# Kernel optimization log

Measured on AMD Instinct MI355X. Metric: run time of the kernel, lower is better.

Reference implementation:

```python
import jax, jax.numpy as jnp
import numpy as np

GAMMA = 0.5
BATCH, DIM, UNITS = 16384, 512, 1024


def setup_inputs() -> dict:
    key = jax.random.key(0)
    k1, k2 = jax.random.split(key)
    inputs = jax.random.normal(k1, (BATCH, DIM), dtype=jnp.float32)
    mu = jax.random.normal(k2, (DIM, UNITS), dtype=jnp.float32)
    return {"inputs": inputs, "mu": mu}


def reference(inputs, mu):
    # Squared L2 distance from each input row to each center (column of mu):
    x_sq = jnp.sum(inputs * inputs, axis=1, keepdims=True)        # [B, 1]
    mu_sq = jnp.sum(mu * mu, axis=0, keepdims=True)               # [1, U]
    cross = inputs @ mu                                           # [B, U] GEMM
    l2 = x_sq - 2.0 * cross + mu_sq                                # [B, U]
    return jnp.exp(-GAMMA * l2)
```

## Files before the change

### kernel.cpp

```cpp
#include <hip/hip_runtime.h>
#include <hip/hip_bf16.h>

#define BATCH 16384
#define DIM   512
#define UNITS 1024

typedef float v16f __attribute__((ext_vector_type(16)));

#define APITCH 516
#define BPITCH 33

__global__ __launch_bounds__(256)
void prep_kernel(const float* __restrict__ in, const float* __restrict__ mu,
                 unsigned char* __restrict__ A8f, unsigned char* __restrict__ B8f,
                 float* __restrict__ xsq, float* __restrict__ musq) {
    __shared__ __attribute__((aligned(16))) char smem[512 * BPITCH * 4 + 1024];
    const int t  = threadIdx.x;
    const int l  = t & 63, w = t >> 6;
    const int ln = l & 31, h = l >> 5;

    if (blockIdx.x < BATCH / 32) {
        float* lds = (float*)smem;
        float* red = (float*)(smem + 32 * APITCH * 4);
        const int c = blockIdx.x;
        const float4* src = (const float4*)(in + (size_t)c * 32 * DIM);
        float4* l4 = (float4*)lds;
#pragma unroll
        for (int i = 0; i < 16; i++) {
            const int f = i * 256 + t;
            l4[(f >> 7) * (APITCH / 4) + (f & 127)] = src[f];
        }
        __syncthreads();
        float s = 0.f;
#pragma unroll
        for (int j = 0; j < 8; j++) {
            const int kw = w * 8 + j;
            const float* p = lds + ln * APITCH + kw * 16 + h * 8;
            float4 f0 = *(const float4*)p;
            float4 f1 = *(const float4*)(p + 4);
            s += f0.x * f0.x + f0.y * f0.y + f0.z * f0.z + f0.w * f0.w
               + f1.x * f1.x + f1.y * f1.y + f1.z * f1.z + f1.w * f1.w;
            int lo = __builtin_amdgcn_cvt_pk_fp8_f32(f0.x, f0.y, 0, false);
            lo     = __builtin_amdgcn_cvt_pk_fp8_f32(f0.z, f0.w, lo, true);
            int hi = __builtin_amdgcn_cvt_pk_fp8_f32(f1.x, f1.y, 0, false);
            hi     = __builtin_amdgcn_cvt_pk_fp8_f32(f1.z, f1.w, hi, true);
            *(int2*)(A8f + (((size_t)c * 32 + kw) * 64 + l) * 8) = make_int2(lo, hi);
        }
        red[ln * 8 + w * 2 + h] = s;
        __syncthreads();
        if (t < 32) {
            float a = 0.f;
#pragma unroll
            for (int i = 0; i < 8; i++) a += red[t * 8 + i];
            xsq[c * 32 + t] = a;
        }
    } else {
        float* lds = (float*)smem;
        float* red = (float*)(smem + 512 * BPITCH * 4);
        const int nb = blockIdx.x - BATCH / 32;
        const int n0 = nb * 32;
        const int col = t & 31, kg = t >> 5;
        float s = 0.f;
        for (int i = 0; i < 64; i++) {
            const int k = i * 8 + kg;
            float v = mu[(size_t)k * UNITS + n0 + col];
            s += v * v;
            lds[k * BPITCH + col] = v;
        }
        red[col * 8 + kg] = s;
        __syncthreads();
        if (t < 32) {
            float a = 0.f;
#pragma unroll
            for (int i = 0; i < 8; i++) a += red[t * 8 + i];
            musq[n0 + t] = a;
        }
#pragma unroll
        for (int j = 0; j < 8; j++) {
            const int kw = w * 8 + j;
            const float* p = lds + (kw * 16 + h * 8) * BPITCH + ln;
            float f[8];
#pragma unroll
            for (int i = 0; i < 8; i++) f[i] = p[i * BPITCH];
            int lo = __builtin_amdgcn_cvt_pk_fp8_f32(f[0], f[1], 0, false);
            lo     = __builtin_amdgcn_cvt_pk_fp8_f32(f[2], f[3], lo, true);
            int hi = __builtin_amdgcn_cvt_pk_fp8_f32(f[4], f[5], 0, false);
            hi     = __builtin_amdgcn_cvt_pk_fp8_f32(f[6], f[7], hi, true);
            *(int2*)(B8f + (((size_t)nb * 32 + kw) * 64 + l) * 8) = make_int2(lo, hi);
        }
    }
}

__global__ __launch_bounds__(256, 2)
void rbf_gemm_kernel(const unsigned char* __restrict__ A8f,
                     const unsigned char* __restrict__ B8f,
                     const float* __restrict__ xsq,
                     const float* __restrict__ musq,
                     float* __restrict__ out) {
    const int t  = threadIdx.x;
    const int l  = t & 63;
    const int w  = t >> 6;
    const int ln = l & 31;
    const int h  = l >> 5;

    const int b  = blockIdx.x;
    const int x  = b & 7;
    const int q  = b >> 3;
    const int rg = q & 15;
    const int cg = q >> 4;
    const int m0 = x * 2048 + rg * 128;
    const int ng = cg * 4 + w;
    const int chunk0 = m0 >> 5;

    const long* Af = (const long*)A8f + ((size_t)chunk0 * 32) * 64 + l;
    const long* Bf = (const long*)B8f + ((size_t)ng * 32) * 64 + l;

    v16f acc[4];
#pragma unroll
    for (int c = 0; c < 4; c++) acc[c] = (v16f)0.f;

#pragma unroll 8
    for (int kw = 0; kw < 32; kw++) {
        long bk = Bf[kw * 64];
        long a0 = Af[(0 * 32 + kw) * 64];
        long a1 = Af[(1 * 32 + kw) * 64];
        long a2 = Af[(2 * 32 + kw) * 64];
        long a3 = Af[(3 * 32 + kw) * 64];
        acc[0] = __builtin_amdgcn_mfma_f32_32x32x16_fp8_fp8(a0, bk, acc[0], 0, 0, 0);
        acc[1] = __builtin_amdgcn_mfma_f32_32x32x16_fp8_fp8(a1, bk, acc[1], 0, 0, 0);
        acc[2] = __builtin_amdgcn_mfma_f32_32x32x16_fp8_fp8(a2, bk, acc[2], 0, 0, 0);
        acc[3] = __builtin_amdgcn_mfma_f32_32x32x16_fp8_fp8(a3, bk, acc[3], 0, 0, 0);
    }

    const float mb = -0.5f * musq[ng * 32 + ln];
#pragma unroll
    for (int c = 0; c < 4; c++) {
#pragma unroll
        for (int r = 0; r < 16; r++) {
            const int rl  = (r & 3) + 8 * (r >> 2) + 4 * h;
            const int row = m0 + c * 32 + rl;
            float v = __expf(acc[c][r] - 0.5f * xsq[row] + mb);
            __builtin_nontemporal_store(v, out + (size_t)row * UNITS + ng * 32 + ln);
        }
    }
}

extern "C" void kernel_launch(void* const* d_in, const int* in_sizes, int n_in,
                              void* d_out, int out_size, void* d_ws, size_t ws_size,
                              hipStream_t stream) {
    const float* inputs = (const float*)d_in[0];
    const float* mu     = (const float*)d_in[1];
    float* out = (float*)d_out;

    char* ws = (char*)d_ws;
    unsigned char* A8f = (unsigned char*)ws;
    unsigned char* B8f = (unsigned char*)(ws + (size_t)BATCH * DIM);
    float* xsq  = (float*)(ws + (size_t)BATCH * DIM + (size_t)UNITS * DIM);
    float* musq = xsq + BATCH;

    prep_kernel<<<BATCH / 32 + UNITS / 32, 256, 0, stream>>>(
        inputs, mu, A8f, B8f, xsq, musq);
    rbf_gemm_kernel<<<1024, 256, 0, stream>>>(A8f, B8f, xsq, musq, out);
}
```

Baseline: 116.6 us.

## Use 2x2 per-wave MFMA tiles, shuffle xsq, raise occupancy, reorder prep blocks

```diff
diff --git a/kernel.cpp b/kernel.cpp
--- a/kernel.cpp
+++ b/kernel.cpp
@@ -19,10 +19,10 @@
     const int l  = t & 63, w = t >> 6;
     const int ln = l & 31, h = l >> 5;
 
-    if (blockIdx.x < BATCH / 32) {
+    if (blockIdx.x >= UNITS / 32) {
         float* lds = (float*)smem;
         float* red = (float*)(smem + 32 * APITCH * 4);
-        const int c = blockIdx.x;
+        const int c = blockIdx.x - UNITS / 32;
         const float4* src = (const float4*)(in + (size_t)c * 32 * DIM);
         float4* l4 = (float4*)lds;
 #pragma unroll
@@ -57,7 +57,7 @@
     } else {
         float* lds = (float*)smem;
         float* red = (float*)(smem + 512 * BPITCH * 4);
-        const int nb = blockIdx.x - BATCH / 32;
+        const int nb = blockIdx.x;
         const int n0 = nb * 32;
         const int col = t & 31, kg = t >> 5;
         float s = 0.f;
@@ -91,7 +91,7 @@
     }
 }
 
-__global__ __launch_bounds__(256, 2)
+__global__ __launch_bounds__(256, 4)
 void rbf_gemm_kernel(const unsigned char* __restrict__ A8f,
                      const unsigned char* __restrict__ B8f,
                      const float* __restrict__ xsq,
@@ -108,39 +108,46 @@
     const int q  = b >> 3;
     const int rg = q & 15;
     const int cg = q >> 4;
-    const int m0 = x * 2048 + rg * 128;
-    const int ng = cg * 4 + w;
-    const int chunk0 = m0 >> 5;
+    const int m0 = x * 2048 + rg * 128 + (w >> 1) * 64;
+    const int n0 = cg * 128 + (w & 1) * 64;
 
-    const long* Af = (const long*)A8f + ((size_t)chunk0 * 32) * 64 + l;
-    const long* Bf = (const long*)B8f + ((size_t)ng * 32) * 64 + l;
+    const long* Af = (const long*)A8f + (size_t)(m0 >> 5) * 2048 + l;
+    const long* Bf = (const long*)B8f + (size_t)(n0 >> 5) * 2048 + l;
 
-    v16f acc[4];
+    v16f acc[2][2];
 #pragma unroll
-    for (int c = 0; c < 4; c++) acc[c] = (v16f)0.f;
+    for (int c = 0; c < 2; c++)
+#pragma unroll
+        for (int j = 0; j < 2; j++) acc[c][j] = (v16f)0.f;
 
-#pragma unroll 8
+#pragma unroll 4
     for (int kw = 0; kw < 32; kw++) {
-        long bk = Bf[kw * 64];
-        long a0 = Af[(0 * 32 + kw) * 64];
-        long a1 = Af[(1 * 32 + kw) * 64];
-        long a2 = Af[(2 * 32 + kw) * 64];
-        long a3 = Af[(3 * 32 + kw) * 64];
-        acc[0] = __builtin_amdgcn_mfma_f32_32x32x16_fp8_fp8(a0, bk, acc[0], 0, 0, 0);
-        acc[1] = __builtin_amdgcn_mfma_f32_32x32x16_fp8_fp8(a1, bk, acc[1], 0, 0, 0);
-        acc[2] = __builtin_amdgcn_mfma_f32_32x32x16_fp8_fp8(a2, bk, acc[2], 0, 0, 0);
-        acc[3] = __builtin_amdgcn_mfma_f32_32x32x16_fp8_fp8(a3, bk, acc[3], 0, 0, 0);
+        long a0 = Af[kw * 64];
+        long a1 = Af[2048 + kw * 64];
+        long b0 = Bf[kw * 64];
+        long b1 = Bf[2048 + kw * 64];
+        acc[0][0] = __builtin_amdgcn_mfma_f32_32x32x16_fp8_fp8(a0, b0, acc[0][0], 0, 0, 0);
+        acc[0][1] = __builtin_amdgcn_mfma_f32_32x32x16_fp8_fp8(a0, b1, acc[0][1], 0, 0, 0);
+        acc[1][0] = __builtin_amdgcn_mfma_f32_32x32x16_fp8_fp8(a1, b0, acc[1][0], 0, 0, 0);
+        acc[1][1] = __builtin_amdgcn_mfma_f32_32x32x16_fp8_fp8(a1, b1, acc[1][1], 0, 0, 0);
     }
 
-    const float mb = -0.5f * musq[ng * 32 + ln];
 #pragma unroll
-    for (int c = 0; c < 4; c++) {
+    for (int c = 0; c < 2; c++) {
+        const int mc = m0 + c * 32;
+        const float xv = -0.5f * xsq[mc + ln];
 #pragma unroll
-        for (int r = 0; r < 16; r++) {
-            const int rl  = (r & 3) + 8 * (r >> 2) + 4 * h;
-            const int row = m0 + c * 32 + rl;
-            float v = __expf(acc[c][r] - 0.5f * xsq[row] + mb);
-            __builtin_nontemporal_store(v, out + (size_t)row * UNITS + ng * 32 + ln);
+        for (int j = 0; j < 2; j++) {
+            const int nc = n0 + j * 32;
+            const float mb = -0.5f * musq[nc + ln];
+#pragma unroll
+            for (int r = 0; r < 16; r++) {
+                const int rl = (r & 3) + 8 * (r >> 2) + 4 * h;
+                const float xb = __shfl(xv, rl, 64);
+                float v = __expf(acc[c][j][r] + xb + mb);
+                __builtin_nontemporal_store(
+                    v, out + (size_t)(mc + rl) * UNITS + nc + ln);
+            }
         }
     }
 }
@@ -158,7 +165,7 @@
     float* xsq  = (float*)(ws + (size_t)BATCH * DIM + (size_t)UNITS * DIM);
     float* musq = xsq + BATCH;
 
-    prep_kernel<<<BATCH / 32 + UNITS / 32, 256, 0, stream>>>(
+    prep_kernel<<<UNITS / 32 + BATCH / 32, 256, 0, stream>>>(
         inputs, mu, A8f, B8f, xsq, musq);
     rbf_gemm_kernel<<<1024, 256, 0, stream>>>(A8f, B8f, xsq, musq, out);
 }
```

New measurement: 117.6 us. No clear change (+0.9%).
